# Kernel optimization log

Measured on AMD Instinct MI355X. Metric: run time of the kernel, lower is better.

Reference implementation:

```python
import jax, jax.numpy as jnp
import numpy as np

TAU = 0.5
LOGIT_TAU = float(np.log(TAU / (1.0 - TAU)))  # = 0.0 for tau=0.5
N_STEPS = 128           # torch samples randint(128,129) -> always 128
N_SECANT = 8
D_MIN, D_MAX = 0.0, 2.4
B, N, HID, CDIM = 4, 8192, 64, 128


def decoder(p, c, W1, Wc, b1, W2, b2):
    """Occupancy-logit MLP. p: (B, ..., 3), c: (B, CDIM) -> (B, ...)."""
    cc = c @ Wc  # (B, HID)
    cc = cc.reshape(cc.shape[:1] + (1,) * (p.ndim - 2) + cc.shape[1:])
    h = jax.nn.relu(jnp.einsum('...d,dh->...h', p, W1) + cc + b1)
    return (h @ W2 + b2)[..., 0]


def setup_inputs() -> dict:
    key = jax.random.key(0)
    ks = jax.random.split(key, 8)
    return {
        'ray0': jax.random.normal(ks[0], (B, N, 3), jnp.float32) * 0.5,
        'ray_direction': jax.random.normal(ks[1], (B, N, 3), jnp.float32),
        'c': jax.random.normal(ks[2], (B, CDIM), jnp.float32),
        'W1': jax.random.normal(ks[3], (3, HID), jnp.float32) * 0.5,
        'Wc': jax.random.normal(ks[4], (CDIM, HID), jnp.float32) * 0.1,
        'b1': jax.random.normal(ks[5], (HID,), jnp.float32) * 0.1,
        'W2': jax.random.normal(ks[6], (HID, 1), jnp.float32) * 0.5,
        'b2': jax.random.normal(ks[7], (1,), jnp.float32) * 0.1,
    }


def reference(ray0, ray_direction, c, W1, Wc, b1, W2, b2):
    S = N_STEPS
    bsz, npts, _ = ray0.shape
    dec = lambda p: decoder(p, c, W1, Wc, b1, W2, b2)

    # --- coarse ray marching ---
    d_prop = jnp.linspace(D_MIN, D_MAX, S).astype(ray0.dtype)        # (S,)
    p_prop = ray0[:, :, None, :] + ray_direction[:, :, None, :] * d_prop[None, None, :, None]
    val = dec(p_prop) - LOGIT_TAU                                    # (B, N, S)

    mask_0_not_occupied = val[:, :, 0] < 0
    sign_matrix = jnp.concatenate(
        [jnp.sign(val[:, :, :-1] * val[:, :, 1:]),
         jnp.ones((bsz, npts, 1), val.dtype)], axis=-1)
    cost_matrix = sign_matrix * jnp.arange(S, 0, -1, dtype=val.dtype)
    indices = jnp.argmin(cost_matrix, axis=-1)                       # (B, N)
    values = jnp.min(cost_matrix, axis=-1)
    mask_sign_change = values < 0
    f_low = jnp.take_along_axis(val, indices[..., None], axis=2)[..., 0]
    mask_neg_to_pos = f_low < 0
    mask = mask_sign_change & mask_neg_to_pos & mask_0_not_occupied

    d_prop_full = jnp.broadcast_to(d_prop, (bsz, npts, S))
    d_low = jnp.take_along_axis(d_prop_full, indices[..., None], axis=2)[..., 0]
    idx_hi = jnp.minimum(indices + 1, S - 1)
    d_high = jnp.take_along_axis(d_prop_full, idx_hi[..., None], axis=2)[..., 0]
    f_high = jnp.take_along_axis(val, idx_hi[..., None], axis=2)[..., 0]

    # safe placeholders for non-surface rays (results discarded by mask)
    d_low = jnp.where(mask, d_low, 0.0)
    d_high = jnp.where(mask, d_high, 1.0)
    f_low = jnp.where(mask, f_low, -1.0)
    f_high = jnp.where(mask, f_high, 1.0)

    # --- secant refinement (vectorized over all rays) ---
    d_pred = -f_low * (d_high - d_low) / (f_high - f_low) + d_low
    for _ in range(N_SECANT):
        p_mid = ray0 + d_pred[..., None] * ray_direction
        f_mid = dec(p_mid) - LOGIT_TAU
        ind_low = f_mid < 0
        d_low = jnp.where(ind_low, d_pred, d_low)
        f_low = jnp.where(ind_low, f_mid, f_low)
        d_high = jnp.where(ind_low, d_high, d_pred)
        f_high = jnp.where(ind_low, f_high, f_mid)
        d_pred = -f_low * (d_high - d_low) / (f_high - f_low) + d_low

    d_out = jnp.where(mask, d_pred, jnp.inf)
    d_out = jnp.where(mask_0_not_occupied, d_out, 0.0)
    return d_out
```

## Files before the change

### kernel.cpp

```cpp
#include <hip/hip_runtime.h>
#include <hip/hip_bf16.h>

#define HID   64
#define CDIM  128
#define NSTEP 128
#define NRAYS 32768

typedef const __hip_bfloat16* __restrict__ bf16p;

#define WS_CCB  0
#define WS_WX   256
#define WS_WY   320
#define WS_WZ   384
#define WS_W2   448
#define WS_CNT  512
#define WS_DTAB 640
#define QID     1024
#define QDL     (QID + 32768)
#define QDH     (QDL + 32768)
#define QFL     (QDH + 32768)
#define QFH     (QFL + 32768)

__device__ __forceinline__ float bf2f(__hip_bfloat16 x) { return __bfloat162float(x); }

__global__ void precompute_cc(bf16p c, bf16p Wc, bf16p b1, bf16p W1, bf16p W2,
                              float* __restrict__ ws) {
    __shared__ float part[4][HID];
    const float STEPF = 2.4f / 127.0f;
    int b = blockIdx.x;
    int h = threadIdx.x & 63;
    int q = threadIdx.x >> 6;
    float acc = 0.0f;
    const __hip_bfloat16* crow = c + b * CDIM;
#pragma unroll
    for (int k = q * 32; k < q * 32 + 32; ++k)
        acc = fmaf(bf2f(crow[k]), bf2f(Wc[k * HID + h]), acc);
    part[q][h] = acc;
    if (b == 0) {
        if (q == 1) {
            ws[WS_WX + h] = bf2f(W1[h]);
            ws[WS_WY + h] = bf2f(W1[HID + h]);
        } else if (q == 2) {
            ws[WS_WZ + h] = bf2f(W1[2 * HID + h]);
            ws[WS_W2 + h] = bf2f(W2[h]);
        } else if (q == 3) {
            if (h < 4) ((int*)ws)[WS_CNT + h] = 0;
            ws[WS_DTAB + h]      = bf2f(__float2bfloat16((float)h * STEPF));
            ws[WS_DTAB + 64 + h] = bf2f(__float2bfloat16((float)(h + 64) * STEPF));
        }
    }
    __syncthreads();
    if (q == 0)
        ws[WS_CCB + b * HID + h] =
            bf2f(b1[h]) + ((part[0][h] + part[1][h]) + (part[2][h] + part[3][h]));
}

__global__ __launch_bounds__(256) void raymarch(
    bf16p ray0, bf16p rdir, bf16p b2,
    float* __restrict__ ws, __hip_bfloat16* __restrict__ out) {
    __shared__ float4 sABW[4][HID][4];

    const int tid  = threadIdx.x;
    const int wave = tid >> 6;
    const int lane = tid & 63;
    const int rbase = blockIdx.x * 16 + wave * 4;
    const int batch = blockIdx.x >> 9;

    const float b2v = bf2f(b2[0]);
    const float STEPF = 2.4f / 127.0f;

    {
        const float wx  = ws[WS_WX + lane];
        const float wy  = ws[WS_WY + lane];
        const float wz  = ws[WS_WZ + lane];
        const float w2l = ws[WS_W2 + lane];
        const float cb  = ws[WS_CCB + batch * HID + lane];
#pragma unroll
        for (int t = 0; t < 4; ++t) {
            const int r = rbase + t;
            const float ox = bf2f(ray0[r * 3 + 0]), oy = bf2f(ray0[r * 3 + 1]), oz = bf2f(ray0[r * 3 + 2]);
            const float dx = bf2f(rdir[r * 3 + 0]), dy = bf2f(rdir[r * 3 + 1]), dz = bf2f(rdir[r * 3 + 2]);
            float a  = fmaf(ox, wx, fmaf(oy, wy, fmaf(oz, wz, cb)));
            float bb = fmaf(dx, wx, fmaf(dy, wy, dz * wz));
            sABW[wave][lane][t] = make_float4(a, bb, w2l, 0.0f);
        }
    }

    const int t = lane >> 4;
    const int g = lane & 15;

    const float4 dt0 = *(const float4*)(ws + WS_DTAB + 8 * g);
    const float4 dt1 = *(const float4*)(ws + WS_DTAB + 8 * g + 4);
    float d[8] = {dt0.x, dt0.y, dt0.z, dt0.w, dt1.x, dt1.y, dt1.z, dt1.w};
    float v[8];
#pragma unroll
    for (int k = 0; k < 8; ++k) v[k] = b2v;

    const float4* __restrict__ abw = &sABW[wave][0][t];
#pragma unroll
    for (int j = 0; j < HID; ++j) {
        const float4 ab = abw[j * 4];
#pragma unroll
        for (int k = 0; k < 8; ++k) {
            float h = fmaf(d[k], ab.y, ab.x);
            v[k] = fmaf(fmaxf(h, 0.0f), ab.z, v[k]);
        }
    }

    float nv = __shfl_down(v[0], 1);
    float key;
#pragma unroll
    for (int k = 0; k < 8; ++k) {
        const int s = 8 * g + k;
        float vn = (k < 7) ? v[k + 1] : nv;
        float prod = v[k] * vn;
        float sgn = (prod < 0.0f) ? -1.0f : ((prod > 0.0f) ? 1.0f : 0.0f);
        float kk = (s == NSTEP - 1) ? (256.0f + 127.0f)
                                    : fmaf(sgn * (float)(NSTEP - s), 256.0f, (float)s);
        key = (k == 0) ? kk : fminf(key, kk);
    }
#pragma unroll
    for (int off = 1; off < 16; off <<= 1)
        key = fminf(key, __shfl_xor(key, off));
    const float cf = floorf(key * 0.00390625f);
    const int   mi = (int)(key - cf * 256.0f);

    const int idx  = mi;
    const int idxh = (idx + 1 < NSTEP) ? idx + 1 : NSTEP - 1;
    const int q  = idx  & 7, qh = idxh & 7;

    float cand = v[0], candh = v[0];
#pragma unroll
    for (int k = 1; k < 8; ++k) {
        cand  = (q  == k) ? v[k] : cand;
        candh = (qh == k) ? v[k] : candh;
    }
    const int lane_lo = (lane & 48) | (idx  >> 3);
    const int lane_hi = (lane & 48) | (idxh >> 3);
    float f_low  = __shfl(cand,  lane_lo);
    float f_high = __shfl(candh, lane_hi);
    float v00    = __shfl(v[0], lane & 48);

    bool m0   = v00 < 0.0f;
    bool mask = (key < 0.0f) && (f_low < 0.0f) && m0;

    if (g == 0) {
        const int r = rbase + t;
        if (mask) {
            int pos = atomicAdd((int*)ws + WS_CNT + batch, 1);
            int qo  = batch * 8192 + pos;
            ((int*)ws)[QID + qo] = r;
            ws[QDL + qo] = bf2f(__float2bfloat16(idx  * STEPF));
            ws[QDH + qo] = bf2f(__float2bfloat16(idxh * STEPF));
            ws[QFL + qo] = f_low;
            ws[QFH + qo] = f_high;
        } else {
            out[r] = __float2bfloat16(m0 ? 0x1.FEp127f : 0.0f);
        }
    }
}

__global__ __launch_bounds__(256) void secant(
    bf16p ray0, bf16p rdir, bf16p b2,
    const float* __restrict__ ws, __hip_bfloat16* __restrict__ out) {
    __shared__ float4 sW4[HID];
    __shared__ float  sCB[HID];

    const int gtid  = blockIdx.x * 256 + threadIdx.x;
    const int batch = gtid >> 13;
    const int i     = gtid & 8191;

    if (threadIdx.x < HID) {
        int j = threadIdx.x;
        sW4[j] = make_float4(ws[WS_WX + j], ws[WS_WY + j], ws[WS_WZ + j], ws[WS_W2 + j]);
        sCB[j] = ws[WS_CCB + batch * HID + j];
    }
    __syncthreads();

    const int cnt = ((const int*)ws)[WS_CNT + batch];
    if (i >= cnt) return;

    const int qo  = batch * 8192 + i;
    const int rid = ((const int*)ws)[QID + qo];
    float dl = ws[QDL + qo], dh = ws[QDH + qo];
    float fl = ws[QFL + qo], fh = ws[QFH + qo];

    const float ox = bf2f(ray0[rid * 3 + 0]), oy = bf2f(ray0[rid * 3 + 1]), oz = bf2f(ray0[rid * 3 + 2]);
    const float dx = bf2f(rdir[rid * 3 + 0]), dy = bf2f(rdir[rid * 3 + 1]), dz = bf2f(rdir[rid * 3 + 2]);
    const float b2v = bf2f(b2[0]);

    float dp = -fl * (dh - dl) / (fh - fl) + dl;
#pragma unroll
    for (int it = 0; it < 8; ++it) {
        float px = fmaf(dp, dx, ox), py = fmaf(dp, dy, oy), pz = fmaf(dp, dz, oz);
        float acc = b2v;
#pragma unroll 8
        for (int j = 0; j < HID; ++j) {
            float4 w = sW4[j];
            float h = fmaf(px, w.x, fmaf(py, w.y, fmaf(pz, w.z, sCB[j])));
            acc = fmaf(fmaxf(h, 0.0f), w.w, acc);
        }
        bool lowside = acc < 0.0f;
        dl = lowside ? dp : dl;
        fl = lowside ? acc : fl;
        dh = lowside ? dh : dp;
        fh = lowside ? fh : acc;
        dp = -fl * (dh - dl) / (fh - fl) + dl;
    }
    out[rid] = __float2bfloat16(dp);
}

extern "C" void kernel_launch(void* const* d_in, const int* in_sizes, int n_in,
                              void* d_out, int out_size, void* d_ws, size_t ws_size,
                              hipStream_t stream) {
    bf16p ray0 = (bf16p)d_in[0];
    bf16p rdir = (bf16p)d_in[1];
    bf16p c    = (bf16p)d_in[2];
    bf16p W1   = (bf16p)d_in[3];
    bf16p Wc   = (bf16p)d_in[4];
    bf16p b1   = (bf16p)d_in[5];
    bf16p W2   = (bf16p)d_in[6];
    bf16p b2   = (bf16p)d_in[7];
    __hip_bfloat16* out = (__hip_bfloat16*)d_out;
    float* ws = (float*)d_ws;

    hipLaunchKernelGGL(precompute_cc, dim3(4), dim3(256), 0, stream, c, Wc, b1, W1, W2, ws);
    hipLaunchKernelGGL(raymarch, dim3(NRAYS / 16), dim3(256), 0, stream,
                       ray0, rdir, b2, ws, out);
    hipLaunchKernelGGL(secant, dim3(128), dim3(256), 0, stream,
                       ray0, rdir, b2, ws, out);
}
```

Before: 90.21 us.

## Replace per-step MLP evaluation with piecewise-linear difference-array prefix scan

Along a ray, each hidden unit's ReLU is linear in depth with a single kink at -alpha/beta. The coarse march now drops the 64-unit loop per step: it finds each unit's kink step, scatters its slope and intercept contributions into a shared-memory difference array with LDS atomics, then prefix-scans to get the decoder value at every step as A+B*d. This cuts the arithmetic from HID times steps to roughly HID plus steps per ray, at the cost of shared atomics, a scan, and rounding that differs from direct evaluation, which could flip sign decisions near zero.

```diff
diff --git a/kernel.cpp b/kernel.cpp
--- a/kernel.cpp
+++ b/kernel.cpp
@@ -21,12 +21,15 @@
 #define QFL     (QDH + 32768)
 #define QFH     (QFL + 32768)
 
+#define STEPF   (2.4f / 127.0f)
+#define INVSTEP (127.0f / 2.4f)
+#define DENT 144
+
 __device__ __forceinline__ float bf2f(__hip_bfloat16 x) { return __bfloat162float(x); }
 
 __global__ void precompute_cc(bf16p c, bf16p Wc, bf16p b1, bf16p W1, bf16p W2,
                               float* __restrict__ ws) {
     __shared__ float part[4][HID];
-    const float STEPF = 2.4f / 127.0f;
     int b = blockIdx.x;
     int h = threadIdx.x & 63;
     int q = threadIdx.x >> 6;
@@ -58,7 +61,7 @@
 __global__ __launch_bounds__(256) void raymarch(
     bf16p ray0, bf16p rdir, bf16p b2,
     float* __restrict__ ws, __hip_bfloat16* __restrict__ out) {
-    __shared__ float4 sABW[4][HID][4];
+    __shared__ __align__(16) float2 sD[4][4][DENT];
 
     const int tid  = threadIdx.x;
     const int wave = tid >> 6;
@@ -67,7 +70,13 @@
     const int batch = blockIdx.x >> 9;
 
     const float b2v = bf2f(b2[0]);
-    const float STEPF = 2.4f / 127.0f;
+
+    {
+        float2* z = &sD[wave][0][0];
+#pragma unroll
+        for (int i = 0; i < 9; ++i)
+            z[lane + 64 * i] = make_float2(0.0f, 0.0f);
+    }
 
     {
         const float wx  = ws[WS_WX + lane];
@@ -80,32 +89,82 @@
             const int r = rbase + t;
             const float ox = bf2f(ray0[r * 3 + 0]), oy = bf2f(ray0[r * 3 + 1]), oz = bf2f(ray0[r * 3 + 2]);
             const float dx = bf2f(rdir[r * 3 + 0]), dy = bf2f(rdir[r * 3 + 1]), dz = bf2f(rdir[r * 3 + 2]);
-            float a  = fmaf(ox, wx, fmaf(oy, wy, fmaf(oz, wz, cb)));
-            float bb = fmaf(dx, wx, fmaf(dy, wy, dz * wz));
-            sABW[wave][lane][t] = make_float4(a, bb, w2l, 0.0f);
+            const float alpha = fmaf(ox, wx, fmaf(oy, wy, fmaf(oz, wz, cb)));
+            const float beta  = fmaf(dx, wx, fmaf(dy, wy, dz * wz));
+            const float ap = alpha * w2l;
+            const float bp = beta  * w2l;
+
+#if __has_builtin(__builtin_amdgcn_rcpf)
+            float td = -alpha * __builtin_amdgcn_rcpf(beta);
+#else
+            float td = -alpha / beta;
+#endif
+            float sf = floorf(td * INVSTEP) + 1.0f;
+            sf = fminf(fmaxf(sf, 1.0f), 128.0f);
+            const int si = (int)sf;
+            const int t1 = si - 1;
+            const int t2 = (si < 127) ? si : 127;
+            const float d1 = bf2f(__float2bfloat16((float)t1 * STEPF));
+            const float d2 = bf2f(__float2bfloat16((float)t2 * STEPF));
+            const bool bpos = beta > 0.0f;
+            const bool p1 = (fmaf(d1, beta, alpha) > 0.0f) == bpos;
+            const bool p2 = (fmaf(d2, beta, alpha) > 0.0f) == bpos;
+            int sc = p1 ? t1 : (p2 ? si : si + 1);
+            sc = (sc < 128) ? sc : 128;
+            int sb, se; bool do_b, do_e;
+            if (beta == 0.0f) { sb = 0;  do_b = (alpha > 0.0f); se = 0;  do_e = false; }
+            else if (bpos)    { sb = sc; do_b = (sc < 128);     se = 0;  do_e = false; }
+            else              { sb = 0;  do_b = (sc > 0);       se = sc; do_e = (sc < 128); }
+            float2* base = &sD[wave][t][0];
+            const int slot_b = (sb == 0) ? (130 + (lane & 7)) : sb;
+            if (do_b) {
+                atomicAdd(&base[slot_b].x, ap);
+                atomicAdd(&base[slot_b].y, bp);
+            }
+            if (do_e) {
+                atomicAdd(&base[se].x, -ap);
+                atomicAdd(&base[se].y, -bp);
+            }
         }
     }
 
     const int t = lane >> 4;
     const int g = lane & 15;
 
+    const float4* rp = (const float4*)&sD[wave][t][8 * g];
+    const float4 q0 = rp[0], q1 = rp[1], q2 = rp[2], q3 = rp[3];
+    float A[8], Bv[8];
+    A[0] = q0.x;        Bv[0] = q0.y;
+    A[1] = A[0] + q0.z; Bv[1] = Bv[0] + q0.w;
+    A[2] = A[1] + q1.x; Bv[2] = Bv[1] + q1.y;
+    A[3] = A[2] + q1.z; Bv[3] = Bv[2] + q1.w;
+    A[4] = A[3] + q2.x; Bv[4] = Bv[3] + q2.y;
+    A[5] = A[4] + q2.z; Bv[5] = Bv[4] + q2.w;
+    A[6] = A[5] + q3.x; Bv[6] = Bv[5] + q3.y;
+    A[7] = A[6] + q3.z; Bv[7] = Bv[6] + q3.w;
+
+    float sAi = A[7], sBi = Bv[7];
+#pragma unroll
+    for (int off = 1; off < 16; off <<= 1) {
+        float aa = __shfl_up(sAi, off, 16);
+        float bb = __shfl_up(sBi, off, 16);
+        sAi += (g >= off) ? aa : 0.0f;
+        sBi += (g >= off) ? bb : 0.0f;
+    }
+    const float4* zp = (const float4*)&sD[wave][t][130];
+    const float4 z0 = zp[0], z1 = zp[1], z2 = zp[2], z3 = zp[3];
+    const float zA = ((z0.x + z0.z) + (z1.x + z1.z)) + ((z2.x + z2.z) + (z3.x + z3.z));
+    const float zB = ((z0.y + z0.w) + (z1.y + z1.w)) + ((z2.y + z2.w) + (z3.y + z3.w));
+    const float baseA = ((sAi - A[7]) + zA) + b2v;
+    const float baseB = (sBi - Bv[7]) + zB;
+
     const float4 dt0 = *(const float4*)(ws + WS_DTAB + 8 * g);
     const float4 dt1 = *(const float4*)(ws + WS_DTAB + 8 * g + 4);
-    float d[8] = {dt0.x, dt0.y, dt0.z, dt0.w, dt1.x, dt1.y, dt1.z, dt1.w};
+    const float d[8] = {dt0.x, dt0.y, dt0.z, dt0.w, dt1.x, dt1.y, dt1.z, dt1.w};
     float v[8];
 #pragma unroll
-    for (int k = 0; k < 8; ++k) v[k] = b2v;
-
-    const float4* __restrict__ abw = &sABW[wave][0][t];
-#pragma unroll
-    for (int j = 0; j < HID; ++j) {
-        const float4 ab = abw[j * 4];
-#pragma unroll
-        for (int k = 0; k < 8; ++k) {
-            float h = fmaf(d[k], ab.y, ab.x);
-            v[k] = fmaf(fmaxf(h, 0.0f), ab.z, v[k]);
-        }
-    }
+    for (int k = 0; k < 8; ++k)
+        v[k] = fmaf(d[k], baseB + Bv[k], baseA + A[k]);
 
     float nv = __shfl_down(v[0], 1);
     float key;
```

Result: slower. 97.63 us (+8.2%).

## Fold W2 into first-layer weights, split hidden units by sign, widen per-lane steps

Applied to the files above, without the earlier changes.

Precompute folds W2 into W1 and the conditioning bias. This works because relu(h)*w = sign(w)*relu(h*|w|)... more precisely, scaling by w2 keeps the relu correct for positive w2 and flips it for negative w2. The hidden units are sorted by the sign of W2, so the raymarch inner loop becomes a fma plus max plus add or subtract, dropping one operand load and the multiply. Each lane now evaluates 16 steps instead of 8 and each block handles 32 rays, which halves the grid and changes the shuffle reductions. The rescaled weights and the different summation order can change rounding near the sign-change decisions, and the higher register count per lane may reduce occupancy.

```diff
diff --git a/kernel.cpp b/kernel.cpp
--- a/kernel.cpp
+++ b/kernel.cpp
@@ -14,19 +14,25 @@
 #define WS_WZ   384
 #define WS_W2   448
 #define WS_CNT  512
+#define WS_NPOS 516
 #define WS_DTAB 640
-#define QID     1024
+#define WS_PWX  768
+#define WS_PWY  832
+#define WS_PWZ  896
+#define WS_PCB  960
+#define QID     2048
 #define QDL     (QID + 32768)
 #define QDH     (QDL + 32768)
 #define QFL     (QDH + 32768)
 #define QFH     (QFL + 32768)
 
+#define STEPF (2.4f / 127.0f)
+
 __device__ __forceinline__ float bf2f(__hip_bfloat16 x) { return __bfloat162float(x); }
 
 __global__ void precompute_cc(bf16p c, bf16p Wc, bf16p b1, bf16p W1, bf16p W2,
                               float* __restrict__ ws) {
     __shared__ float part[4][HID];
-    const float STEPF = 2.4f / 127.0f;
     int b = blockIdx.x;
     int h = threadIdx.x & 63;
     int q = threadIdx.x >> 6;
@@ -50,69 +56,96 @@
         }
     }
     __syncthreads();
-    if (q == 0)
-        ws[WS_CCB + b * HID + h] =
-            bf2f(b1[h]) + ((part[0][h] + part[1][h]) + (part[2][h] + part[3][h]));
+    if (q == 0) {
+        float cb = bf2f(b1[h]) + ((part[0][h] + part[1][h]) + (part[2][h] + part[3][h]));
+        ws[WS_CCB + b * HID + h] = cb;
+        float w2h = bf2f(W2[h]);
+        unsigned long long m = __ballot(w2h >= 0.0f);
+        int npos = __popcll(m);
+        unsigned long long lower = (1ull << h) - 1ull;
+        int posrank = __popcll(m & lower);
+        int rank = (w2h >= 0.0f) ? posrank : (npos + (h - posrank));
+        ws[WS_PCB + b * HID + rank] = cb * w2h;
+        if (b == 0) {
+            ws[WS_PWX + rank] = bf2f(W1[h]) * w2h;
+            ws[WS_PWY + rank] = bf2f(W1[HID + h]) * w2h;
+            ws[WS_PWZ + rank] = bf2f(W1[2 * HID + h]) * w2h;
+            if (h == 0) ((int*)ws)[WS_NPOS] = npos;
+        }
+    }
 }
 
 __global__ __launch_bounds__(256) void raymarch(
     bf16p ray0, bf16p rdir, bf16p b2,
     float* __restrict__ ws, __hip_bfloat16* __restrict__ out) {
-    __shared__ float4 sABW[4][HID][4];
+    __shared__ float2 sAB[4 * HID * 8 + 8];
 
     const int tid  = threadIdx.x;
     const int wave = tid >> 6;
     const int lane = tid & 63;
-    const int rbase = blockIdx.x * 16 + wave * 4;
-    const int batch = blockIdx.x >> 9;
+    const int rbase = blockIdx.x * 32 + wave * 8;
+    const int batch = blockIdx.x >> 8;
 
     const float b2v = bf2f(b2[0]);
-    const float STEPF = 2.4f / 127.0f;
 
     {
-        const float wx  = ws[WS_WX + lane];
-        const float wy  = ws[WS_WY + lane];
-        const float wz  = ws[WS_WZ + lane];
-        const float w2l = ws[WS_W2 + lane];
-        const float cb  = ws[WS_CCB + batch * HID + lane];
-#pragma unroll
-        for (int t = 0; t < 4; ++t) {
+        const float wx = ws[WS_PWX + lane];
+        const float wy = ws[WS_PWY + lane];
+        const float wz = ws[WS_PWZ + lane];
+        const float cb = ws[WS_PCB + batch * HID + lane];
+#pragma unroll
+        for (int t = 0; t < 8; ++t) {
             const int r = rbase + t;
             const float ox = bf2f(ray0[r * 3 + 0]), oy = bf2f(ray0[r * 3 + 1]), oz = bf2f(ray0[r * 3 + 2]);
             const float dx = bf2f(rdir[r * 3 + 0]), dy = bf2f(rdir[r * 3 + 1]), dz = bf2f(rdir[r * 3 + 2]);
             float a  = fmaf(ox, wx, fmaf(oy, wy, fmaf(oz, wz, cb)));
             float bb = fmaf(dx, wx, fmaf(dy, wy, dz * wz));
-            sABW[wave][lane][t] = make_float4(a, bb, w2l, 0.0f);
-        }
-    }
-
-    const int t = lane >> 4;
-    const int g = lane & 15;
-
-    const float4 dt0 = *(const float4*)(ws + WS_DTAB + 8 * g);
-    const float4 dt1 = *(const float4*)(ws + WS_DTAB + 8 * g + 4);
-    float d[8] = {dt0.x, dt0.y, dt0.z, dt0.w, dt1.x, dt1.y, dt1.z, dt1.w};
-    float v[8];
-#pragma unroll
-    for (int k = 0; k < 8; ++k) v[k] = b2v;
-
-    const float4* __restrict__ abw = &sABW[wave][0][t];
-#pragma unroll
-    for (int j = 0; j < HID; ++j) {
-        const float4 ab = abw[j * 4];
-#pragma unroll
-        for (int k = 0; k < 8; ++k) {
+            sAB[(wave * HID + lane) * 8 + t] = make_float2(a, bb);
+        }
+    }
+
+    const int t = lane >> 3;
+    const int g = lane & 7;
+
+    const float* dt = ws + WS_DTAB + 16 * g;
+    const float4 A0 = ((const float4*)dt)[0], A1 = ((const float4*)dt)[1];
+    const float4 A2 = ((const float4*)dt)[2], A3 = ((const float4*)dt)[3];
+    const float d[16] = {A0.x, A0.y, A0.z, A0.w, A1.x, A1.y, A1.z, A1.w,
+                         A2.x, A2.y, A2.z, A2.w, A3.x, A3.y, A3.z, A3.w};
+    float v[16];
+#pragma unroll
+    for (int k = 0; k < 16; ++k) v[k] = b2v;
+
+    const int npos = __builtin_amdgcn_readfirstlane(((const int*)ws)[WS_NPOS]);
+    const float2* __restrict__ pbase = &sAB[wave * HID * 8 + t];
+
+    float2 ab = pbase[0];
+    int j = 0;
+    for (; j < npos; ++j) {
+        float2 nx = pbase[8 * (j + 1)];
+#pragma unroll
+        for (int k = 0; k < 16; ++k) {
             float h = fmaf(d[k], ab.y, ab.x);
-            v[k] = fmaf(fmaxf(h, 0.0f), ab.z, v[k]);
-        }
+            v[k] += fmaxf(h, 0.0f);
+        }
+        ab = nx;
+    }
+    for (; j < HID; ++j) {
+        float2 nx = pbase[8 * (j + 1)];
+#pragma unroll
+        for (int k = 0; k < 16; ++k) {
+            float h = fmaf(d[k], ab.y, ab.x);
+            v[k] -= fmaxf(h, 0.0f);
+        }
+        ab = nx;
     }
 
     float nv = __shfl_down(v[0], 1);
     float key;
 #pragma unroll
-    for (int k = 0; k < 8; ++k) {
-        const int s = 8 * g + k;
-        float vn = (k < 7) ? v[k + 1] : nv;
+    for (int k = 0; k < 16; ++k) {
+        const int s = 16 * g + k;
+        float vn = (k < 15) ? v[k + 1] : nv;
         float prod = v[k] * vn;
         float sgn = (prod < 0.0f) ? -1.0f : ((prod > 0.0f) ? 1.0f : 0.0f);
         float kk = (s == NSTEP - 1) ? (256.0f + 127.0f)
@@ -120,26 +153,26 @@
         key = (k == 0) ? kk : fminf(key, kk);
     }
 #pragma unroll
-    for (int off = 1; off < 16; off <<= 1)
+    for (int off = 1; off < 8; off <<= 1)
         key = fminf(key, __shfl_xor(key, off));
     const float cf = floorf(key * 0.00390625f);
     const int   mi = (int)(key - cf * 256.0f);
 
     const int idx  = mi;
     const int idxh = (idx + 1 < NSTEP) ? idx + 1 : NSTEP - 1;
-    const int q  = idx  & 7, qh = idxh & 7;
+    const int q  = idx  & 15, qh = idxh & 15;
 
     float cand = v[0], candh = v[0];
 #pragma unroll
-    for (int k = 1; k < 8; ++k) {
+    for (int k = 1; k < 16; ++k) {
         cand  = (q  == k) ? v[k] : cand;
         candh = (qh == k) ? v[k] : candh;
     }
-    const int lane_lo = (lane & 48) | (idx  >> 3);
-    const int lane_hi = (lane & 48) | (idxh >> 3);
+    const int lane_lo = (lane & 56) | (idx  >> 4);
+    const int lane_hi = (lane & 56) | (idxh >> 4);
     float f_low  = __shfl(cand,  lane_lo);
     float f_high = __shfl(candh, lane_hi);
-    float v00    = __shfl(v[0], lane & 48);
+    float v00    = __shfl(v[0], lane & 56);
 
     bool m0   = v00 < 0.0f;
     bool mask = (key < 0.0f) && (f_low < 0.0f) && m0;
@@ -225,7 +258,7 @@
     float* ws = (float*)d_ws;
 
     hipLaunchKernelGGL(precompute_cc, dim3(4), dim3(256), 0, stream, c, Wc, b1, W1, W2, ws);
-    hipLaunchKernelGGL(raymarch, dim3(NRAYS / 16), dim3(256), 0, stream,
+    hipLaunchKernelGGL(raymarch, dim3(NRAYS / 32), dim3(256), 0, stream,
                        ray0, rdir, b2, ws, out);
     hipLaunchKernelGGL(secant, dim3(128), dim3(256), 0, stream,
                        ray0, rdir, b2, ws, out);
```

New measurement: 103.1 us. 1.14x slower.
